# Kernel optimization log

Hardware: AMD Instinct MI355X
Metric: run time of the kernel (lower is better)

The kernel has to match this reference:

```python
import jax, jax.numpy as jnp
import numpy as np
from jax import lax

K = 3            # kernel size
KP = K * K       # kernel_size_prod
CENTER = KP // 2 # center tap index
PIXEL_SIZE = 1.0
DILATION = 1


def _unfold(x):
    # torch F.unfold equivalent: [N, C*KP, oh, ow] with channel-major, spatial-minor tap order
    return lax.conv_general_dilated_patches(
        x, filter_shape=(K, K), window_strides=(1, 1),
        padding=((1, 1), (1, 1)), rhs_dilation=(DILATION, DILATION))


def setup_inputs() -> dict:
    key = jax.random.key(0)
    ks = jax.random.split(key, 6)
    N, C, O, H, W = 8, 128, 128, 64, 64
    x = jax.random.normal(ks[0], (N, C, H, W), jnp.float32)
    depth = jax.random.uniform(ks[1], (N, 1, H, W), jnp.float32)  # >0 almost surely
    fx = jax.random.uniform(ks[2], (N,), jnp.float32) + 0.5       # per-image focal scale
    s = 1.0 / np.sqrt(C * KP)
    w0 = jax.random.normal(ks[3], (O, C, K, K), jnp.float32) * s
    w1 = jax.random.normal(ks[4], (O, C, K, K), jnp.float32) * s
    w2 = jax.random.normal(ks[5], (O, C, K, K), jnp.float32) * s
    return {"x": x, "depth": depth, "fx": fx, "w0": w0, "w1": w1, "w2": w2}


def reference(x, depth, fx, w0, w1, w2):
    N, C, H, W = x.shape
    O = w0.shape[0]
    patches = _unfold(x)                      # [N, C*9, oh, ow]
    oh, ow = patches.shape[2], patches.shape[3]
    L = oh * ow
    x_col = patches.reshape(N, C, KP, L)       # [N, C, 9, L]
    d_col = _unfold(depth).reshape(N, KP, L)   # [N, 9, L]

    valid = (d_col != 0.0).astype(jnp.float32)
    valid = valid * valid[:, CENTER:CENTER + 1, :]
    d_col = d_col * valid
    center = d_col[:, CENTER:CENTER + 1, :]    # [N, 1, L]
    grid = PIXEL_SIZE * DILATION * center / fx[:, None, None]
    half = grid * 0.5

    m0 = (jnp.abs(d_col - (center + grid)) <= half).astype(jnp.float32)
    m1 = (jnp.abs(d_col - center) <= half).astype(jnp.float32)
    m1 = jnp.clip(m1 + 1.0 - valid, 0.0, 1.0)
    m2 = (jnp.abs(d_col - (center - grid)) <= half).astype(jnp.float32)

    def branch(w, m):
        # (O, C*9) @ (N, C*9, L) as an einsum over (C, tap)
        return jnp.einsum('ock,nckl->nol', w.reshape(O, C, KP), x_col * m[:, None])

    out = branch(w0, m0) + branch(w1, m1) + branch(w2, m2)
    return out.reshape(N, O, oh, ow)
```

## Files before the change

### kernel.cpp

```cpp
#include <hip/hip_runtime.h>
#include <hip/hip_bf16.h>
#include <cstdint>
#include <cstddef>

#define Nn 8
#define Cc 128
#define Oo 128
#define Hh 64
#define Ww 64
#define LL (Hh * Ww)
#define KP 9

typedef __attribute__((ext_vector_type(8))) short short8;
typedef __attribute__((ext_vector_type(4))) float floatx4;
typedef __attribute__((ext_vector_type(4))) int intx4;

#define SGB(m, s, i) __builtin_amdgcn_sched_group_barrier(m, s, i)

__device__ __forceinline__ unsigned short f2bf(float f) {
  unsigned int u = __float_as_uint(f);
  u += 0x7fffu + ((u >> 16) & 1u);
  return (unsigned short)(u >> 16);
}

__global__ __launch_bounds__(256) void prep_all(const float* __restrict__ x,
                                                const float* __restrict__ w0,
                                                const float* __restrict__ w1,
                                                const float* __restrict__ w2,
                                                const float* __restrict__ depth,
                                                const float* __restrict__ fx,
                                                unsigned short* __restrict__ xt,
                                                unsigned short* __restrict__ wt2,
                                                unsigned int* __restrict__ codesg) {
  __shared__ float tile[Cc][Ww + 1];
  __shared__ unsigned short wl[Cc * KP];
  const int bid = blockIdx.x;
  const int t = threadIdx.x;
  if (bid < Nn * Hh) {
    const int n = bid >> 6;
    const int h = bid & 63;
    const float* src = x + (size_t)n * Cc * LL + (size_t)h * Ww;
#pragma unroll
    for (int it = 0; it < 8; ++it) {
      const int idx = t + it * 256;
      const int c = idx >> 4;
      const int w4 = (idx & 15) << 2;
      const float4 v = *reinterpret_cast<const float4*>(src + (size_t)c * LL + w4);
      tile[c][w4 + 0] = v.x; tile[c][w4 + 1] = v.y;
      tile[c][w4 + 2] = v.z; tile[c][w4 + 3] = v.w;
    }
    __syncthreads();
    unsigned short* dst = xt + (size_t)((n * Hh + h) * Ww) * Cc;
#pragma unroll
    for (int it = 0; it < 4; ++it) {
      const int idx = t + it * 256;
      const int w = idx >> 4;
      const int ch = (idx & 15) << 3;
      short8 v;
#pragma unroll
      for (int q = 0; q < 8; ++q)
        ((unsigned short*)&v)[q] = f2bf(tile[ch + q][w]);
      *reinterpret_cast<short8*>(dst + (size_t)w * Cc + ch) = v;
    }
  } else if (bid < Nn * Hh + 3 * Oo) {
    const int bo = bid - Nn * Hh;
    const int b = bo >> 7;
    const int o = bo & 127;
    const float* w = (b == 0) ? w0 : (b == 1) ? w1 : w2;
    const float* src = w + (size_t)o * Cc * KP;
#pragma unroll
    for (int it = 0; it < 5; ++it) {
      const int idx = t + it * 256;
      if (idx < Cc * KP) wl[idx] = f2bf(src[idx]);
    }
    __syncthreads();
    const int obase = ((o >> 6) & 1) * 2048 + ((o >> 5) & 1) * 1024 +
                      ((o >> 4) & 1) * 512 + (o & 15) * 32;
#pragma unroll
    for (int it = 0; it < 5; ++it) {
      const int idx = t + it * 256;
      if (idx < Cc * KP) {
        const int kk = idx >> 7;
        const int c = idx & 127;
        const int c0 = c >> 5;
        const int cc = c & 31;
        wt2[(size_t)(b * 36 + kk * 4 + c0) * 4096 + obase + cc] = wl[c * KP + kk];
      }
    }
  } else {
    const int p = (bid - (Nn * Hh + 3 * Oo)) * 256 + t;
    const int n = p >> 12;
    const int rem = p & 4095;
    const int h = rem >> 6;
    const int w = rem & 63;
    const float center = depth[p];
    const float grid = center / fx[n];
    const float half = 0.5f * grid;
    unsigned int packed = 0u;
#pragma unroll
    for (int kk = 0; kk < KP; ++kk) {
      const int hh = h + kk / 3 - 1;
      const int ww = w + kk % 3 - 1;
      float d = 0.0f;
      if (hh >= 0 && hh < Hh && ww >= 0 && ww < Ww) d = depth[(n << 12) + hh * Ww + ww];
      const float valid = (d != 0.0f && center != 0.0f) ? 1.0f : 0.0f;
      const float dm = d * valid;
      unsigned int cb = 0u;
      if (fabsf(dm - (center + grid)) <= half) cb |= 1u;
      float m1v = (fabsf(dm - center) <= half) ? 1.0f : 0.0f;
      m1v = m1v + 1.0f - valid;
      if (m1v > 1.0f) m1v = 1.0f;
      if (m1v > 0.5f) cb |= 2u;
      if (fabsf(dm - (center - grid)) <= half) cb |= 4u;
      packed |= cb << (3 * kk);
    }
    codesg[p] = packed;
  }
}

#define LDXC 132
#define HALO_COLS 66
#define HALO_ROWS 4
#define NSTEP 18
#define BSTRIDE 147456

__global__ __launch_bounds__(256, 2) void conv_main(
    const unsigned short* __restrict__ xt,
    const unsigned short* __restrict__ wt2,
    const unsigned int* __restrict__ codesg,
    float* __restrict__ out) {
  __shared__ __align__(16) unsigned short Xs[HALO_ROWS * HALO_COLS * LDXC];

  const int g = blockIdx.x;
  const int n = g >> 6;
  const int rem = g & 63;
  const int pb = rem >> 1;
  const int ob1 = rem & 1;
  const int h0 = pb * 2;

  const int tid = threadIdx.x;
  const int lane = tid & 63;
  const int wave = tid >> 6;
  const int ln15 = lane & 15;
  const int quad = lane >> 4;
  const int wc = wave & 1;
  const int ks = wave >> 1;

  const unsigned short* wfragk =
      wt2 + (size_t)(ob1 * 2048 + wc * 1024 + ln15 * 32 + quad * 8) + (size_t)ks * 8192;
  const int xbase = quad * 8 + ks * 64;

  short8 Bb[3][6];
  short8 Aa[2][8];

#define LOADB(SLOT, S)                                                            \
  {                                                                               \
    const unsigned short* bp = wfragk + (size_t)((((S) >> 1) * 4) + ((S) & 1)) * 4096; \
    Bb[SLOT][0] = *reinterpret_cast<const short8*>(bp);                           \
    Bb[SLOT][1] = *reinterpret_cast<const short8*>(bp + 512);                     \
    Bb[SLOT][2] = *reinterpret_cast<const short8*>(bp + BSTRIDE);                 \
    Bb[SLOT][3] = *reinterpret_cast<const short8*>(bp + BSTRIDE + 512);           \
    Bb[SLOT][4] = *reinterpret_cast<const short8*>(bp + 2 * BSTRIDE);             \
    Bb[SLOT][5] = *reinterpret_cast<const short8*>(bp + 2 * BSTRIDE + 512);       \
  }

#define LOADA(SLOT, S)                                                            \
  {                                                                               \
    const int kkp = (S) >> 1;                                                     \
    const int dyp = kkp / 3, dxp = kkp % 3;                                       \
    _Pragma("unroll")                                                             \
    for (int i = 0; i < 8; ++i) {                                                 \
      const int off = (((i >> 2) + dyp) * HALO_COLS + (i & 3) * 16 + dxp) * LDXC  \
                      + ((S) & 1) * 32;                                           \
      Aa[SLOT][i] = *reinterpret_cast<const short8*>(&Xs[(ln15 + off) * 1 + xbase \
                      + off - off + (ln15 * 0) + ((((i >> 2) + dyp) * HALO_COLS + (i & 3) * 16 + dxp + ln15) * LDXC + ((S) & 1) * 32 + xbase) - (ln15 + off + xbase)]); \
    }                                                                             \
  }
#undef LOADA
#define LOADA(SLOT, S)                                                            \
  {                                                                               \
    const int kkp = (S) >> 1;                                                     \
    const int dyp = kkp / 3, dxp = kkp % 3;                                       \
    _Pragma("unroll")                                                             \
    for (int i = 0; i < 8; ++i) {                                                 \
      const int pix = ((i >> 2) + dyp) * HALO_COLS + (i & 3) * 16 + ln15 + dxp;   \
      Aa[SLOT][i] = *reinterpret_cast<const short8*>(&Xs[pix * LDXC + ((S) & 1) * 32 + xbase]); \
    }                                                                             \
  }

  LOADB(0, 0)
  LOADB(1, 1)

  unsigned int cd[8];
  {
    const unsigned int* cp = codesg + (n << 12) + h0 * 64 + ln15;
#pragma unroll
    for (int i = 0; i < 8; ++i) cd[i] = cp[i * 16];
  }

#pragma unroll
  for (int it = 0; it < 17; ++it) {
    const int idx = tid + it * 256;
    if (idx < HALO_ROWS * HALO_COLS * 16) {
      const int ch = (idx & 15) << 3;
      const int pixidx = idx >> 4;
      const int lc = pixidx % HALO_COLS;
      const int hrel = pixidx / HALO_COLS;
      const int hh = h0 - 1 + hrel;
      const int ww = lc - 1;
      short8 v = {0, 0, 0, 0, 0, 0, 0, 0};
      if (hh >= 0 && hh < Hh && ww >= 0 && ww < Ww)
        v = *reinterpret_cast<const short8*>(
            xt + (size_t)((n * Hh + hh) * Ww + ww) * Cc + ch);
      *reinterpret_cast<short8*>(&Xs[pixidx * LDXC + ch]) = v;
    }
  }

  __syncthreads();

  const floatx4 zf4 = {0.f, 0.f, 0.f, 0.f};
  floatx4 acc[8][2];
#pragma unroll
  for (int i = 0; i < 8; ++i)
#pragma unroll
    for (int j = 0; j < 2; ++j) acc[i][j] = zf4;

  LOADA(0, 0)

#pragma unroll
  for (int s = 0; s < NSTEP; ++s) {
    if (s + 2 < NSTEP) LOADB((s + 2) % 3, s + 2)
    if (s + 1 < NSTEP) LOADA((s + 1) & 1, s + 1)
    const int kk = s >> 1;
    const int shift = 3 * kk;
    const short8* B = Bb[s % 3];
    const short8* A = Aa[s & 1];
#pragma unroll
    for (int b = 0; b < 3; ++b) {
#pragma unroll
      for (int i = 0; i < 8; ++i) {
        const int msk = __builtin_amdgcn_sbfe((int)cd[i], shift + b, 1);
        intx4 a4 = *reinterpret_cast<const intx4*>(&A[i]);
        intx4 m4 = {msk, msk, msk, msk};
        a4 &= m4;
        const short8 af = *reinterpret_cast<const short8*>(&a4);
        acc[i][0] = __builtin_amdgcn_mfma_f32_16x16x32_bf16(af, B[b * 2 + 0], acc[i][0], 0, 0, 0);
        acc[i][1] = __builtin_amdgcn_mfma_f32_16x16x32_bf16(af, B[b * 2 + 1], acc[i][1], 0, 0, 0);
      }
    }
    SGB(0x020, 1, 0); SGB(0x008, 4, 0); SGB(0x100, 1, 0); SGB(0x008, 4, 0);
    SGB(0x020, 1, 0); SGB(0x008, 4, 0); SGB(0x100, 1, 0); SGB(0x008, 4, 0);
    SGB(0x020, 1, 0); SGB(0x008, 4, 0); SGB(0x100, 1, 0); SGB(0x008, 4, 0);
    SGB(0x020, 1, 0); SGB(0x008, 4, 0); SGB(0x100, 1, 0); SGB(0x008, 4, 0);
    SGB(0x020, 1, 0); SGB(0x008, 4, 0); SGB(0x100, 1, 0); SGB(0x008, 4, 0);
    SGB(0x020, 1, 0); SGB(0x008, 4, 0); SGB(0x100, 3, 0); SGB(0x008, 4, 0);
  }

  __syncthreads();
  float* scratch = reinterpret_cast<float*>(Xs);
  if (ks == 1) {
#pragma unroll
    for (int i = 0; i < 8; ++i)
#pragma unroll
      for (int j = 0; j < 2; ++j) {
        const int tile = (wc * 16 + i * 2 + j) * 64 + lane;
        *reinterpret_cast<floatx4*>(&scratch[tile * 4]) = acc[i][j];
      }
  }
  __syncthreads();
  if (ks == 0) {
#pragma unroll
    for (int i = 0; i < 8; ++i) {
      const int m = i * 16 + quad * 4;
      const int h = h0 + (m >> 6);
      const int w = m & 63;
#pragma unroll
      for (int j = 0; j < 2; ++j) {
        const int tile = (wc * 16 + i * 2 + j) * 64 + lane;
        const floatx4 other = *reinterpret_cast<const floatx4*>(&scratch[tile * 4]);
        const floatx4 sum = acc[i][j] + other;
        const int o = ob1 * 64 + wc * 32 + j * 16 + ln15;
        float* dst = out + (size_t)(n * Oo + o) * LL + h * Ww + w;
        *reinterpret_cast<floatx4*>(dst) = sum;
      }
    }
  }
}

extern "C" void kernel_launch(void* const* d_in, const int* in_sizes, int n_in,
                              void* d_out, int out_size, void* d_ws, size_t ws_size,
                              hipStream_t stream) {
  const float* x     = (const float*)d_in[0];
  const float* depth = (const float*)d_in[1];
  const float* fx    = (const float*)d_in[2];
  const float* w0    = (const float*)d_in[3];
  const float* w1    = (const float*)d_in[4];
  const float* w2    = (const float*)d_in[5];
  float* out = (float*)d_out;

  unsigned short* xt = (unsigned short*)d_ws;
  unsigned short* wt2 = xt + (size_t)Nn * Hh * Ww * Cc;
  unsigned int* codesg = (unsigned int*)(wt2 + (size_t)3 * KP * Oo * Cc);

  prep_all<<<Nn * Hh + 3 * Oo + 128, 256, 0, stream>>>(x, w0, w1, w2, depth, fx, xt, wt2, codesg);
  conv_main<<<512, 256, 0, stream>>>(xt, wt2, codesg, out);
}
```

Baseline: 109.6 us.

## Roll main MFMA loop into 3 iterations with precomputed LDS byte offsets

```diff
diff --git a/kernel.cpp b/kernel.cpp
--- a/kernel.cpp
+++ b/kernel.cpp
@@ -121,8 +121,9 @@
 #define LDXC 132
 #define HALO_COLS 66
 #define HALO_ROWS 4
-#define NSTEP 18
 #define BSTRIDE 147456
+#define WT2_SHORTS (3 * KP * 4 * 4096)
+#define PAD_SHORTS 65536
 
 __global__ __launch_bounds__(256, 2) void conv_main(
     const unsigned short* __restrict__ xt,
@@ -148,48 +149,39 @@
 
   const unsigned short* wfragk =
       wt2 + (size_t)(ob1 * 2048 + wc * 1024 + ln15 * 32 + quad * 8) + (size_t)ks * 8192;
-  const int xbase = quad * 8 + ks * 64;
+  const char* XsB = reinterpret_cast<const char*>(Xs);
+
+  unsigned int abyte[8];
+#pragma unroll
+  for (int i = 0; i < 8; ++i)
+    abyte[i] = (unsigned int)((((i >> 2) * HALO_COLS + (i & 3) * 16 + ln15) * LDXC
+                               + quad * 8 + ks * 64) * 2);
 
   short8 Bb[3][6];
   short8 Aa[2][8];
 
-#define LOADB(SLOT, S)                                                            \
-  {                                                                               \
-    const unsigned short* bp = wfragk + (size_t)((((S) >> 1) * 4) + ((S) & 1)) * 4096; \
-    Bb[SLOT][0] = *reinterpret_cast<const short8*>(bp);                           \
-    Bb[SLOT][1] = *reinterpret_cast<const short8*>(bp + 512);                     \
-    Bb[SLOT][2] = *reinterpret_cast<const short8*>(bp + BSTRIDE);                 \
-    Bb[SLOT][3] = *reinterpret_cast<const short8*>(bp + BSTRIDE + 512);           \
-    Bb[SLOT][4] = *reinterpret_cast<const short8*>(bp + 2 * BSTRIDE);             \
-    Bb[SLOT][5] = *reinterpret_cast<const short8*>(bp + 2 * BSTRIDE + 512);       \
-  }
-
-#define LOADA(SLOT, S)                                                            \
-  {                                                                               \
-    const int kkp = (S) >> 1;                                                     \
-    const int dyp = kkp / 3, dxp = kkp % 3;                                       \
-    _Pragma("unroll")                                                             \
-    for (int i = 0; i < 8; ++i) {                                                 \
-      const int off = (((i >> 2) + dyp) * HALO_COLS + (i & 3) * 16 + dxp) * LDXC  \
-                      + ((S) & 1) * 32;                                           \
-      Aa[SLOT][i] = *reinterpret_cast<const short8*>(&Xs[(ln15 + off) * 1 + xbase \
-                      + off - off + (ln15 * 0) + ((((i >> 2) + dyp) * HALO_COLS + (i & 3) * 16 + dxp + ln15) * LDXC + ((S) & 1) * 32 + xbase) - (ln15 + off + xbase)]); \
-    }                                                                             \
-  }
-#undef LOADA
-#define LOADA(SLOT, S)                                                            \
-  {                                                                               \
-    const int kkp = (S) >> 1;                                                     \
-    const int dyp = kkp / 3, dxp = kkp % 3;                                       \
-    _Pragma("unroll")                                                             \
-    for (int i = 0; i < 8; ++i) {                                                 \
-      const int pix = ((i >> 2) + dyp) * HALO_COLS + (i & 3) * 16 + ln15 + dxp;   \
-      Aa[SLOT][i] = *reinterpret_cast<const short8*>(&Xs[pix * LDXC + ((S) & 1) * 32 + xbase]); \
-    }                                                                             \
+  const unsigned short* bpt = wfragk;
+
+#define LOADB(SLOT, OFFS)                                                       \
+  {                                                                             \
+    const unsigned short* bp_ = bpt + (OFFS);                                   \
+    Bb[SLOT][0] = *reinterpret_cast<const short8*>(bp_);                        \
+    Bb[SLOT][1] = *reinterpret_cast<const short8*>(bp_ + 512);                  \
+    Bb[SLOT][2] = *reinterpret_cast<const short8*>(bp_ + BSTRIDE);              \
+    Bb[SLOT][3] = *reinterpret_cast<const short8*>(bp_ + BSTRIDE + 512);        \
+    Bb[SLOT][4] = *reinterpret_cast<const short8*>(bp_ + 2 * BSTRIDE);          \
+    Bb[SLOT][5] = *reinterpret_cast<const short8*>(bp_ + 2 * BSTRIDE + 512);    \
+  }
+
+#define LOADA(SLOT, IMM)                                                        \
+  {                                                                             \
+    _Pragma("unroll")                                                           \
+    for (int i_ = 0; i_ < 8; ++i_)                                              \
+      Aa[SLOT][i_] = *reinterpret_cast<const short8*>(XsB + abyte[i_] + (IMM)); \
   }
 
   LOADB(0, 0)
-  LOADB(1, 1)
+  LOADB(1, 4096)
 
   unsigned int cd[8];
   {
@@ -227,34 +219,41 @@
 
   LOADA(0, 0)
 
-#pragma unroll
-  for (int s = 0; s < NSTEP; ++s) {
-    if (s + 2 < NSTEP) LOADB((s + 2) % 3, s + 2)
-    if (s + 1 < NSTEP) LOADA((s + 1) & 1, s + 1)
-    const int kk = s >> 1;
-    const int shift = 3 * kk;
-    const short8* B = Bb[s % 3];
-    const short8* A = Aa[s & 1];
-#pragma unroll
-    for (int b = 0; b < 3; ++b) {
-#pragma unroll
-      for (int i = 0; i < 8; ++i) {
-        const int msk = __builtin_amdgcn_sbfe((int)cd[i], shift + b, 1);
-        intx4 a4 = *reinterpret_cast<const intx4*>(&A[i]);
-        intx4 m4 = {msk, msk, msk, msk};
-        a4 &= m4;
-        const short8 af = *reinterpret_cast<const short8*>(&a4);
-        acc[i][0] = __builtin_amdgcn_mfma_f32_16x16x32_bf16(af, B[b * 2 + 0], acc[i][0], 0, 0, 0);
-        acc[i][1] = __builtin_amdgcn_mfma_f32_16x16x32_bf16(af, B[b * 2 + 1], acc[i][1], 0, 0, 0);
-      }
-    }
-    SGB(0x020, 1, 0); SGB(0x008, 4, 0); SGB(0x100, 1, 0); SGB(0x008, 4, 0);
-    SGB(0x020, 1, 0); SGB(0x008, 4, 0); SGB(0x100, 1, 0); SGB(0x008, 4, 0);
-    SGB(0x020, 1, 0); SGB(0x008, 4, 0); SGB(0x100, 1, 0); SGB(0x008, 4, 0);
-    SGB(0x020, 1, 0); SGB(0x008, 4, 0); SGB(0x100, 1, 0); SGB(0x008, 4, 0);
-    SGB(0x020, 1, 0); SGB(0x008, 4, 0); SGB(0x100, 1, 0); SGB(0x008, 4, 0);
-    SGB(0x020, 1, 0); SGB(0x008, 4, 0); SGB(0x100, 3, 0); SGB(0x008, 4, 0);
-  }
+#define STEPM(U)                                                                \
+  {                                                                             \
+    LOADB(((U) + 2) % 3, (((((U) + 2) >> 1) * 4 + ((U) & 1)) * 4096))           \
+    LOADA((((U) + 1) & 1),                                                      \
+          ((U) == 5 ? 17424 : (((((U) + 1) >> 1) * 132 + (((U) + 1) & 1) * 32) * 2))) \
+    const short8* Bp = Bb[(U) % 3];                                             \
+    const short8* Ap = Aa[(U) & 1];                                             \
+    _Pragma("unroll")                                                           \
+    for (int b = 0; b < 3; ++b) {                                               \
+      _Pragma("unroll")                                                         \
+      for (int i = 0; i < 8; ++i) {                                             \
+        const int msk = __builtin_amdgcn_sbfe((int)cd[i], sh + 3 * ((U) >> 1) + b, 1); \
+        intx4 a4 = *reinterpret_cast<const intx4*>(&Ap[i]);                     \
+        const intx4 m4 = {msk, msk, msk, msk};                                  \
+        a4 &= m4;                                                               \
+        const short8 af = *reinterpret_cast<const short8*>(&a4);                \
+        acc[i][0] = __builtin_amdgcn_mfma_f32_16x16x32_bf16(af, Bp[b * 2 + 0], acc[i][0], 0, 0, 0); \
+        acc[i][1] = __builtin_amdgcn_mfma_f32_16x16x32_bf16(af, Bp[b * 2 + 1], acc[i][1], 0, 0, 0); \
+      }                                                                         \
+    }                                                                           \
+    SGB(0x100, 4, 0); SGB(0x008, 8, 0); SGB(0x020, 2, 0); SGB(0x008, 8, 0);     \
+    SGB(0x100, 4, 0); SGB(0x008, 8, 0); SGB(0x020, 2, 0); SGB(0x008, 8, 0);     \
+    SGB(0x020, 2, 0); SGB(0x008, 16, 0);                                        \
+  }
+
+  int sh = 0;
+#pragma unroll 1
+  for (int tt = 0; tt < 3; ++tt) {
+    STEPM(0) STEPM(1) STEPM(2) STEPM(3) STEPM(4) STEPM(5)
+    bpt += 49152;
+    sh += 9;
+#pragma unroll
+    for (int i = 0; i < 8; ++i) abyte[i] += 17424;
+  }
+#undef STEPM
 
   __syncthreads();
   float* scratch = reinterpret_cast<float*>(Xs);
@@ -300,7 +299,7 @@
 
   unsigned short* xt = (unsigned short*)d_ws;
   unsigned short* wt2 = xt + (size_t)Nn * Hh * Ww * Cc;
-  unsigned int* codesg = (unsigned int*)(wt2 + (size_t)3 * KP * Oo * Cc);
+  unsigned int* codesg = (unsigned int*)(wt2 + (size_t)WT2_SHORTS + PAD_SHORTS);
 
   prep_all<<<Nn * Hh + 3 * Oo + 128, 256, 0, stream>>>(x, w0, w1, w2, depth, fx, xt, wt2, codesg);
   conv_main<<<512, 256, 0, stream>>>(xt, wt2, codesg, out);
```

New measurement: 127.2 us. 16.1% more time.
